# Optimization experiments

Measured on AMD Instinct MI355X. Metric: run time of the kernel, lower is better.

## Reference

```python
import jax, jax.numpy as jnp
import numpy as np

NH = 16   # neighbors
MD = 64   # model_dim
FF = 128  # ff_dim
H = 4     # heads
HD = MD // H
B, S, T = 2, 8192, 4096
LOG100 = float(np.log(100.0))


def _ln(x, g, b, eps=1e-5):
    m = x.mean(-1, keepdims=True)
    v = ((x - m) ** 2).mean(-1, keepdims=True)
    return (x - m) * jax.lax.rsqrt(v + eps) * g + b


def _lrelu(x):
    return jnp.where(x >= 0, x, 0.2 * x)


def setup_inputs():
    ks = jax.random.split(jax.random.key(0), 16)
    rn = lambda k, sh: jax.random.normal(k, sh, dtype=jnp.float32) * 0.05
    return {
        "x": jax.random.normal(ks[0], (B, S, 1), dtype=jnp.float32),
        "c1": jax.random.normal(ks[1], (B, S, T), dtype=jnp.float32),
        "c2": jax.random.normal(ks[2], (B, S, T), dtype=jnp.float32),
        "pe_W1": rn(ks[3], (2, FF)), "pe_b1": jnp.zeros((FF,), jnp.float32),
        "pe_W2": rn(ks[4], (FF, MD)), "pe_b2": jnp.zeros((MD,), jnp.float32),
        "Wq": rn(ks[5], (MD, MD)), "Wk": rn(ks[6], (MD, MD)), "Wv": rn(ks[7], (1, MD)),
        "logit_scale": jnp.full((H, 1, 1), float(np.log(10.0)), jnp.float32),
        "Wo": rn(ks[8], (MD, MD)), "bo": jnp.zeros((MD,), jnp.float32),
        "g1": jnp.ones((MD,), jnp.float32), "beta1": jnp.zeros((MD,), jnp.float32),
        "g2": jnp.ones((MD,), jnp.float32), "beta2": jnp.zeros((MD,), jnp.float32),
        "g3": jnp.ones((MD * NH,), jnp.float32), "beta3": jnp.zeros((MD * NH,), jnp.float32),
        "mnh_W1": rn(ks[9], (MD, FF)), "mnh_b1": jnp.zeros((FF,), jnp.float32),
        "mnh_W2": rn(ks[10], (FF, 1)), "mnh_b2": jnp.zeros((1,), jnp.float32),
        "mu_W1": rn(ks[11], (MD * NH, MD * NH)), "mu_b1": jnp.zeros((MD * NH,), jnp.float32),
        "mu_W2": rn(ks[12], (MD * NH, MD * NH)), "mu_b2": jnp.zeros((MD * NH,), jnp.float32),
    }


def reference(x, c1, c2, pe_W1, pe_b1, pe_W2, pe_b2, Wq, Wk, Wv, logit_scale, Wo, bo,
              g1, beta1, g2, beta2, g3, beta3,
              mnh_W1, mnh_b1, mnh_W2, mnh_b2, mu_W1, mu_b1, mu_W2, mu_b2):
    b, s, t = c1.shape
    # KNN over source axis s (cartesian distance), per target t
    d = c1 * c1 + c2 * c2                                  # [b,s,t]
    _, idx = jax.lax.top_k(-jnp.swapaxes(d, 1, 2), NH)     # [b,t,NH]
    x_nh = jax.vmap(lambda xb, ib: xb[ib])(x, idx)         # [b,t,NH,e]
    c1g = jnp.take_along_axis(jnp.swapaxes(c1, 1, 2), idx, axis=2)  # [b,t,NH]
    c2g = jnp.take_along_axis(jnp.swapaxes(c2, 1, 2), idx, axis=2)
    # relative-position embedding MLP (PE), already in [b,t,NH,MD] layout
    pe = jnp.stack([c1g, c2g], -1)                         # [b,t,NH,2]
    pe = jax.nn.gelu(pe @ pe_W1 + pe_b1) @ pe_W2 + pe_b2   # [b,t,NH,MD]
    h = _ln(x_nh + pe, g1, beta1).reshape(b * t, NH, MD)   # e=1 broadcasts
    v = jnp.einsum('bne,ed->bnd', x_nh.reshape(b * t, NH, 1), Wv)
    q = h @ Wq
    k = h @ Wk
    sp = lambda z: z.reshape(b * t, NH, H, HD).transpose(0, 2, 1, 3)
    qh, kh, vh = sp(q), sp(k), sp(v)
    # logit-scaled (cosine) attention over the NH neighbor axis
    qn = qh * jax.lax.rsqrt(jnp.sum(qh * qh, -1, keepdims=True) + 1e-12)
    kn = kh * jax.lax.rsqrt(jnp.sum(kh * kh, -1, keepdims=True) + 1e-12)
    scale = jnp.exp(jnp.minimum(logit_scale, LOG100))      # [H,1,1]
    att = jax.nn.softmax(jnp.einsum('bhnd,bhmd->bhnm', qn, kn) * scale, axis=-1)
    o = jnp.einsum('bhnm,bhmd->bhnd', att, vh).transpose(0, 2, 1, 3).reshape(b * t, NH, MD)
    h = _ln(h + (o @ Wo + bo), g2, beta2)
    # per-neighbor MLP producing a scalar, broadcast-added back
    h = h + _lrelu(_lrelu(h @ mnh_W1 + mnh_b1) @ mnh_W2 + mnh_b2)
    # unfold neighbors into channels and run the unfold MLP
    h = _ln(h.reshape(b, t, NH * MD), g3, beta3)
    return _lrelu(_lrelu(h @ mu_W1 + mu_b1) @ mu_W2 + mu_b2)  # [b,t,NH*MD]
```

## Files before the change

kernel.cpp:

```cpp
#include <hip/hip_runtime.h>
#include <hip/hip_bf16.h>

#define B_    2
#define SSRC  8192
#define TT    4096
#define NHN   16
#define NC    64
#define CS    128
#define LOG100D 4.605170185988091368035982909368

typedef short s16x8 __attribute__((ext_vector_type(8)));
typedef float f32x4 __attribute__((ext_vector_type(4)));
typedef double f64x4 __attribute__((ext_vector_type(4)));
typedef unsigned long long u64;

typedef const __attribute__((address_space(1))) void* gas_ptr;
typedef __attribute__((address_space(3))) void* las_ptr;
#define GLDS16(g, l) __builtin_amdgcn_global_load_lds((gas_ptr)(g), (las_ptr)(l), 16, 0, 0)

#define WFENCE asm volatile("s_waitcnt lgkmcnt(0)" ::: "memory")

__device__ __forceinline__ unsigned short f2bf(float f) {
    unsigned u = __float_as_uint(f);
    u = u + 0x7fffu + ((u >> 16) & 1u);
    return (unsigned short)(u >> 16);
}
__device__ __forceinline__ float bf2f(unsigned short h) {
    return __uint_as_float(((unsigned)h) << 16);
}
__device__ __forceinline__ double lrelu_d(double v) { return v >= 0.0 ? v : 0.2 * v; }
__device__ __forceinline__ double gelu_d(double u) {
    double a = 0.7978845608028654 * (u + 0.044715 * u * u * u);
    return 0.5 * u * (1.0 + tanh(a));
}
__device__ __forceinline__ double rsum16d(double v) {
    v += __shfl_xor(v, 1); v += __shfl_xor(v, 2);
    v += __shfl_xor(v, 4); v += __shfl_xor(v, 8);
    return v;
}
__device__ __forceinline__ double rmax16d(double v) {
    v = fmax(v, __shfl_xor(v, 1)); v = fmax(v, __shfl_xor(v, 2));
    v = fmax(v, __shfl_xor(v, 4)); v = fmax(v, __shfl_xor(v, 8));
    return v;
}
__device__ __forceinline__ double rsum64d(double v) {
    v += __shfl_xor(v, 1); v += __shfl_xor(v, 2); v += __shfl_xor(v, 4);
    v += __shfl_xor(v, 8); v += __shfl_xor(v, 16); v += __shfl_xor(v, 32);
    return v;
}

__device__ __forceinline__ bool mfma64_probe() {
    int lane = threadIdx.x & 63, l15 = lane & 15, lg = lane >> 4;
    double a = (double)(1 + l15 + 31 * lg);
    double b = (double)(3 + l15 + 17 * lg);
    f64x4 d = (f64x4){0.0, 0.0, 0.0, 0.0};
    d = __builtin_amdgcn_mfma_f64_16x16x4f64(a, b, d, 0, 0, 0);
    bool ok = true;
#pragma unroll
    for (int r = 0; r < 4; r++) {
        int i = 4 * lg + r;
        int e = 0;
#pragma unroll
        for (int k = 0; k < 4; k++) e += (1 + i + 31 * k) * (3 + l15 + 17 * k);
        ok = ok && (d[r] == (double)e);
    }
    return __all(ok) != 0;
}

__device__ __forceinline__ void ce(u64 &a, u64 &b) {
    bool c = a < b; u64 lo = c ? a : b; u64 hi = c ? b : a; a = lo; b = hi;
}
__device__ __forceinline__ void sort16(u64 (&k)[16]) {
    ce(k[0],k[8]); ce(k[1],k[9]); ce(k[2],k[10]); ce(k[3],k[11]);
    ce(k[4],k[12]); ce(k[5],k[13]); ce(k[6],k[14]); ce(k[7],k[15]);
    ce(k[0],k[4]); ce(k[1],k[5]); ce(k[2],k[6]); ce(k[3],k[7]);
    ce(k[8],k[12]); ce(k[9],k[13]); ce(k[10],k[14]); ce(k[11],k[15]);
    ce(k[4],k[8]); ce(k[5],k[9]); ce(k[6],k[10]); ce(k[7],k[11]);
    ce(k[0],k[2]); ce(k[1],k[3]); ce(k[4],k[6]); ce(k[5],k[7]);
    ce(k[8],k[10]); ce(k[9],k[11]); ce(k[12],k[14]); ce(k[13],k[15]);
    ce(k[2],k[8]); ce(k[3],k[9]); ce(k[6],k[12]); ce(k[7],k[13]);
    ce(k[2],k[4]); ce(k[3],k[5]); ce(k[6],k[8]); ce(k[7],k[9]);
    ce(k[10],k[12]); ce(k[11],k[13]);
    ce(k[0],k[1]); ce(k[2],k[3]); ce(k[4],k[5]); ce(k[6],k[7]);
    ce(k[8],k[9]); ce(k[10],k[11]); ce(k[12],k[13]); ce(k[14],k[15]);
    ce(k[1],k[8]); ce(k[3],k[10]); ce(k[5],k[12]); ce(k[7],k[14]);
    ce(k[1],k[4]); ce(k[3],k[6]); ce(k[5],k[8]); ce(k[7],k[10]);
    ce(k[9],k[12]); ce(k[11],k[14]);
    ce(k[1],k[2]); ce(k[3],k[4]); ce(k[5],k[6]); ce(k[7],k[8]);
    ce(k[9],k[10]); ce(k[11],k[12]); ce(k[13],k[14]);
}
__device__ __forceinline__ void bmerge16(u64 (&k)[16]) {
    ce(k[0],k[8]); ce(k[1],k[9]); ce(k[2],k[10]); ce(k[3],k[11]);
    ce(k[4],k[12]); ce(k[5],k[13]); ce(k[6],k[14]); ce(k[7],k[15]);
    ce(k[0],k[4]); ce(k[1],k[5]); ce(k[2],k[6]); ce(k[3],k[7]);
    ce(k[8],k[12]); ce(k[9],k[13]); ce(k[10],k[14]); ce(k[11],k[15]);
    ce(k[0],k[2]); ce(k[1],k[3]); ce(k[4],k[6]); ce(k[5],k[7]);
    ce(k[8],k[10]); ce(k[9],k[11]); ce(k[12],k[14]); ce(k[13],k[15]);
    ce(k[0],k[1]); ce(k[2],k[3]); ce(k[4],k[5]); ce(k[6],k[7]);
    ce(k[8],k[9]); ce(k[10],k[11]); ce(k[12],k[13]); ce(k[14],k[15]);
}
__device__ __forceinline__ void merge_keep16(u64 (&L)[16], const u64 (&B)[16]) {
#pragma unroll
    for (int i = 0; i < 16; i++) { u64 bb = B[15 - i]; L[i] = L[i] < bb ? L[i] : bb; }
    bmerge16(L);
}

__global__ __launch_bounds__(256) void topk_partial(
    const float* __restrict__ c1, const float* __restrict__ c2,
    u64* __restrict__ cand)
{
    int t = blockIdx.x * 256 + threadIdx.x;
    int ch = blockIdx.y, b = blockIdx.z;
    const float* p1 = c1 + ((size_t)b * SSRC + (size_t)ch * CS) * TT + t;
    const float* p2 = c2 + ((size_t)b * SSRC + (size_t)ch * CS) * TT + t;
    u64 k[16];
#pragma unroll
    for (int j = 0; j < 16; j++) k[j] = ~0ull;
    int sbase = ch * CS;
    for (int s = 0; s < CS; s += 16) {
// ... 26 lines not shown
        u64 bt[16];
#pragma unroll
        for (int j = 0; j < 16; j++) bt[j] = src[(size_t)j * TT];
        merge_keep16(k, bt);
    }
    u64* dst = c2c + ((size_t)((b * 8 + g) * 16)) * TT + t;
#pragma unroll
    for (int j = 0; j < 16; j++) dst[(size_t)j * TT] = k[j];
}

__global__ __launch_bounds__(64) void topk_merge2(
    const u64* __restrict__ c2c, int* __restrict__ knn)
{
    int t = blockIdx.x * 64 + threadIdx.x;
    int b = blockIdx.y;
    u64 k[16];
#pragma unroll
    for (int j = 0; j < 16; j++) k[j] = ~0ull;
    for (int c = 0; c < 8; c++) {
        const u64* src = c2c + ((size_t)(b * 8 + c) * 16) * TT + t;
        u64 bt[16];
#pragma unroll
        for (int j = 0; j < 16; j++) bt[j] = src[(size_t)j * TT];
        merge_keep16(k, bt);
    }
#pragma unroll
    for (int j = 0; j < 16; j++)
        knn[((size_t)b * TT + t) * 16 + j] = (int)(unsigned)(k[j] & 0xffffffffull);
}

__global__ __launch_bounds__(256) void wconv(
    const float* __restrict__ Wa, const float* __restrict__ Wb,
    unsigned short* __restrict__ Oah, unsigned short* __restrict__ Oal,
    unsigned short* __restrict__ Obh, unsigned short* __restrict__ Obl)
{
    const float* W = blockIdx.z ? Wb : Wa;
    unsigned short* Oh = blockIdx.z ? Obh : Oah;
    unsigned short* Ol = blockIdx.z ? Obl : Oal;
    __shared__ float tile[64][65];
    int tx = threadIdx.x & 63, ty = threadIdx.x >> 6;
    int n0 = blockIdx.x * 64, k0 = blockIdx.y * 64;
#pragma unroll
    for (int r = ty; r < 64; r += 4) tile[r][tx] = W[(size_t)(k0 + r) * 1024 + n0 + tx];
    __syncthreads();
#pragma unroll
    for (int r = ty; r < 64; r += 4) {
        float v = tile[tx][r];
        unsigned short hi = f2bf(v);
        Oh[(size_t)(n0 + r) * 1024 + k0 + tx] = hi;
        Ol[(size_t)(n0 + r) * 1024 + k0 + tx] = f2bf(v - bf2f(hi));
    }
}

__global__ __launch_bounds__(256) void tok_pe(
    const float* __restrict__ x, const float* __restrict__ c1, const float* __restrict__ c2,
    const int* __restrict__ knn,
    const float* __restrict__ peW1, const float* __restrict__ peb1,
    const float* __restrict__ peW2, const float* __restrict__ peb2,
    const float* __restrict__ g1, const float* __restrict__ be1,
    float* __restrict__ hout)
{
    __shared__ float s_peW1[256], s_peb1[128], s_peW2[8448], s_peb2[64], s_g1[64], s_be1[64];
    __shared__ float s_scr[4][2352];
    int tid = threadIdx.x, lane = tid & 63, w = tid >> 6;
    if (tid < 256) s_peW1[tid] = peW1[tid];
    if (tid < 128) s_peb1[tid] = peb1[tid];
    if (tid < 64) { s_peb2[tid] = peb2[tid]; s_g1[tid] = g1[tid]; s_be1[tid] = be1[tid]; }
    for (int i = tid; i < 8192; i += 256) s_peW2[(i >> 6) * 66 + (i & 63)] = peW2[i];
    __syncthreads();

    bool mf = mfma64_probe();
    float* big = s_scr[w];
    float* sc1 = big + 2304; float* sc2 = big + 2320; float* sx = big + 2336;
    int l15 = lane & 15, lg = lane >> 4;
    double w0a = s_peW1[lane], w1a = s_peW1[128 + lane], ba = s_peb1[lane];
    double w0b = s_peW1[64 + lane], w1b = s_peW1[192 + lane], bbv = s_peb1[64 + lane];
    double gv = (double)s_g1[lane], bv = (double)s_be1[lane];
    double pb2 = (double)s_peb2[lane];
    double g1v[4], be1v[4], pb2v[4];
#pragma unroll
    for (int j = 0; j < 4; j++) {
        g1v[j]  = (double)s_g1[j * 16 + l15];
        be1v[j] = (double)s_be1[j * 16 + l15];
        pb2v[j] = (double)s_peb2[j * 16 + l15];
    }

    for (int it = 0; it < 4; ++it) {
        int tk = blockIdx.x * 16 + w * 4 + it;
        int bb = tk >> 12, tt = tk & (TT - 1);
        if (lane < 16) {
            int s = knn[(size_t)tk * 16 + lane];
            sc1[lane] = c1[((size_t)bb * SSRC + s) * TT + tt];
            sc2[lane] = c2[((size_t)bb * SSRC + s) * TT + tt];
            sx[lane]  = x[bb * SSRC + s];
        }
        WFENCE;
#pragma unroll
        for (int n = 0; n < 16; n++) {
            double a_ = (double)sc1[n], b_ = (double)sc2[n];
            big[lane * 18 + n]        = (float)gelu_d(a_ * w0a + b_ * w1a + ba);
            big[(lane + 64) * 18 + n] = (float)gelu_d(a_ * w0b + b_ * w1b + bbv);
        }
        WFENCE;
        if (mf) {
            f64x4 acc[4];
#pragma unroll
            for (int j = 0; j < 4; j++) acc[j] = (f64x4){0.0, 0.0, 0.0, 0.0};
            for (int ks = 0; ks < 32; ks++) {
                double a = (double)big[(4 * ks + lg) * 18 + l15];
                const float* wrow = &s_peW2[(4 * ks + lg) * 66 + l15];
#pragma unroll
                for (int j = 0; j < 4; j++) {
                    double b = (double)wrow[j * 16];
                    acc[j] = __builtin_amdgcn_mfma_f64_16x16x4f64(a, b, acc[j], 0, 0, 0);
                }
            }
            double xr[4];
#pragma unroll
            for (int r = 0; r < 4; r++) xr[r] = (double)sx[lg * 4 + r];
            float* op = hout + (size_t)tk * 1024;
#pragma unroll
            for (int r = 0; r < 4; r++) {
                double v[4], s = 0.0;
#pragma unroll
                for (int j = 0; j < 4; j++) { v[j] = acc[j][r] + pb2v[j] + xr[r]; s += v[j]; }
                double m = rsum16d(s) * (1.0 / 64.0);
                double q = 0.0;
#pragma unroll
                for (int j = 0; j < 4; j++) { double d = v[j] - m; q += d * d; }
                double var = rsum16d(q) * (1.0 / 64.0);
                double rs = sqrt(var + 1e-5);
                int n = lg * 4 + r;
#pragma unroll
                for (int j = 0; j < 4; j++)
                    op[n * 64 + j * 16 + l15] = (float)((v[j] - m) / rs * g1v[j] + be1v[j]);
            }
        } else {
            double acc[16];
#pragma unroll
            for (int n = 0; n < 16; n++) acc[n] = pb2;
            for (int f = 0; f < 128; f++) {
                double wv = (double)s_peW2[f * 66 + lane];
#pragma unroll
                for (int n = 0; n < 16; n += 2) {
                    float2 gvv = *(const float2*)&big[f * 18 + n];
                    acc[n]     += (double)gvv.x * wv;
                    acc[n + 1] += (double)gvv.y * wv;
                }
            }
            float* op = hout + (size_t)tk * 1024 + lane;
#pragma unroll
            for (int n = 0; n < 16; n++) {
                double v = acc[n] + (double)sx[n];
                double m = rsum64d(v) * (1.0 / 64.0);
                double d = v - m;
                double var = rsum64d(d * d) * (1.0 / 64.0);
                op[n * 64] = (float)(d / sqrt(var + 1e-5) * gv + bv);
            }
        }
    }
}

__global__ __launch_bounds__(256) void tok_attn(
    const float* __restrict__ x, const int* __restrict__ knn,
    const float* __restrict__ Wq, const float* __restrict__ Wk,
    const float* __restrict__ Wv, const float* __restrict__ lsc,
    const float* __restrict__ Wo, const float* __restrict__ bo,
    const float* __restrict__ g2, const float* __restrict__ be2,
    float* __restrict__ hio)
{
    __shared__ float s_Wq[4224], s_Wk[4224], s_WoV[256], s_bo[64], s_g2[64], s_be2[64];
    __shared__ float s_scr[4][2320];
    int tid = threadIdx.x, lane = tid & 63, w = tid >> 6;
    if (tid < 64) {
        s_bo[tid] = bo[tid]; s_g2[tid] = g2[tid]; s_be2[tid] = be2[tid];
        for (int hh = 0; hh < 4; hh++) {
            double a = 0.0;
            for (int hd = 0; hd < 16; hd++)
                a += (double)Wv[hh * 16 + hd] * (double)Wo[(hh * 16 + hd) * 64 + tid];
            s_WoV[hh * 64 + tid] = (float)a;
        }
    }
    for (int i = tid; i < 4096; i += 256) {
        s_Wq[(i >> 6) * 66 + (i & 63)] = Wq[i];
        s_Wk[(i >> 6) * 66 + (i & 63)] = Wk[i];
    }
    __syncthreads();

    bool mf = mfma64_probe();
    int head = lane >> 4, mm = lane & 15;
    int l15 = mm, lg = head;
    double scaleh = exp(fmin((double)lsc[head], LOG100D));
    double wov0 = (double)s_WoV[lane], wov1 = (double)s_WoV[64 + lane];
    double wov2 = (double)s_WoV[128 + lane], wov3 = (double)s_WoV[192 + lane];
    double gv = (double)s_g2[lane], bv = (double)s_be2[lane], bov = (double)s_bo[lane];
    float* big = s_scr[w];
    float* sx = big + 2304;

    for (int it = 0; it < 4; ++it) {
        int tk = blockIdx.x * 16 + w * 4 + it;
        int bb = tk >> 12;
        if (lane < 16) {
            int s = knn[(size_t)tk * 16 + lane];
            sx[lane] = x[bb * SSRC + s];
        }
        float* hp = hio + (size_t)tk * 1024 + lane;
        double h[16];
#pragma unroll
        for (int n = 0; n < 16; n++) {
            h[n] = (double)hp[n * 64];
            big[lane * 18 + n] = (float)h[n];
        }
        WFENCE;
        if (mf) {
            f64x4 qa[4], ka[4];
#pragma unroll
            for (int j = 0; j < 4; j++) { qa[j] = (f64x4){0.,0.,0.,0.}; ka[j] = (f64x4){0.,0.,0.,0.}; }
            for (int ks = 0; ks < 16; ks++) {
                double a = (double)big[(4 * ks + lg) * 18 + l15];
                const float* wq = &s_Wq[(4 * ks + lg) * 66 + l15];
                const float* wk = &s_Wk[(4 * ks + lg) * 66 + l15];
#pragma unroll
                for (int j = 0; j < 4; j++) {
                    qa[j] = __builtin_amdgcn_mfma_f64_16x16x4f64(a, (double)wq[j * 16], qa[j], 0, 0, 0);
                    ka[j] = __builtin_amdgcn_mfma_f64_16x16x4f64(a, (double)wk[j * 16], ka[j], 0, 0, 0);
                }
            }
            WFENCE;
#pragma unroll
            for (int j = 0; j < 4; j++) {
#pragma unroll
                for (int r = 0; r < 4; r++) {
                    double qq = qa[j][r], kk2 = ka[j][r];
                    double sq = rsum16d(qq * qq);
                    double sk = rsum16d(kk2 * kk2);
                    qq  /= sqrt(sq + 1e-12);
                    kk2 /= sqrt(sk + 1e-12);
                    big[(j * 16 + l15) * 18 + 4 * lg + r]        = (float)qq;
                    big[1152 + (j * 16 + l15) * 18 + 4 * lg + r] = (float)kk2;
                }
            }
        } else {
            double q[16], k2[16];
#pragma unroll
            for (int n = 0; n < 16; n++) { q[n] = 0.0; k2[n] = 0.0; }
            for (int kk = 0; kk < 64; kk++) {
                double wq = (double)s_Wq[kk * 66 + lane], wk = (double)s_Wk[kk * 66 + lane];
#pragma unroll
                for (int n = 0; n < 16; n += 2) {
                    float2 hv = *(const float2*)&big[kk * 18 + n];
                    q[n]  += (double)hv.x * wq; q[n + 1]  += (double)hv.y * wq;
                    k2[n] += (double)hv.x * wk; k2[n + 1] += (double)hv.y * wk;
                }
            }
#pragma unroll
            for (int n = 0; n < 16; n++) {
                double sq = rsum16d(q[n] * q[n]);   q[n]  /= sqrt(sq + 1e-12);
                double sk = rsum16d(k2[n] * k2[n]); k2[n] /= sqrt(sk + 1e-12);
            }
            WFENCE;
#pragma unroll
            for (int n = 0; n < 16; n++) {
                big[lane * 18 + n]        = (float)q[n];
                big[1152 + lane * 18 + n] = (float)k2[n];
            }
        }
        WFENCE;
        double A_[16];
        {
            double S[16];
#pragma unroll
            for (int n = 0; n < 16; n++) S[n] = 0.0;
            for (int hd = 0; hd < 16; hd++) {
                int r = head * 16 + hd;
                double kf = (double)big[1152 + r * 18 + mm];
#pragma unroll
                for (int n = 0; n < 16; n += 2) {
                    float2 qq = *(const float2*)&big[r * 18 + n];
                    S[n] += (double)qq.x * kf; S[n + 1] += (double)qq.y * kf;
                }
            }
            double xv = (double)sx[mm];
#pragma unroll
            for (int n = 0; n < 16; n++) {
                double sv = S[n] * scaleh;
                double mx = rmax16d(sv);
                double e = exp(sv - mx);
                double se = rsum16d(e);
                A_[n] = rsum16d((e / se) * xv);
            }
        }
#pragma unroll
        for (int n = 0; n < 16; n++) {
            double a0 = __shfl(A_[n], mm), a1 = __shfl(A_[n], 16 + mm);
            double a2 = __shfl(A_[n], 32 + mm), a3 = __shfl(A_[n], 48 + mm);
            double v = h[n] + a0 * wov0 + a1 * wov1 + a2 * wov2 + a3 * wov3 + bov;
            double m = rsum64d(v) * (1.0 / 64.0);
            double d = v - m;
            double var = rsum64d(d * d) * (1.0 / 64.0);
            hp[n * 64] = (float)(d / sqrt(var + 1e-5) * gv + bv);
        }
    }
}

__global__ __launch_bounds__(256) void tok_mnh(
    const float* __restrict__ hin,
    const float* __restrict__ mW1, const float* __restrict__ mb1,
    const float* __restrict__ mW2, const float* __restrict__ mb2,
    const float* __restrict__ g3, const float* __restrict__ be3,
    unsigned short* __restrict__ hnh, unsigned short* __restrict__ hnl)
{
    __shared__ float s_mW1[8320], s_mb1[128], s_mW2[128], s_g3[1024], s_be3[1024];
    __shared__ float s_scr[4][1152];
    int tid = threadIdx.x, lane = tid & 63, w = tid >> 6;
    if (tid < 128) { s_mb1[tid] = mb1[tid]; s_mW2[tid] = mW2[tid]; }
    for (int i = tid; i < 8192; i += 256) s_mW1[(i >> 7) * 130 + (i & 127)] = mW1[i];
    for (int i = tid; i < 1024; i += 256) { s_g3[i] = g3[i]; s_be3[i] = be3[i]; }
    __syncthreads();

    bool mf = mfma64_probe();
    int l15 = lane & 15, lg = lane >> 4;
    double mb2s = (double)mb2[0];
    double mb1a = (double)s_mb1[lane], mb1b = (double)s_mb1[64 + lane];
    double w2a = (double)s_mW2[lane], w2b = (double)s_mW2[64 + lane];
    double mb1v[8], w2v[8];
#pragma unroll
    for (int j = 0; j < 8; j++) {
        mb1v[j] = (double)s_mb1[j * 16 + l15];
        w2v[j]  = (double)s_mW2[j * 16 + l15];
    }
    float* big = s_scr[w];

    for (int it = 0; it < 4; ++it) {
        int tk = blockIdx.x * 16 + w * 4 + it;
        const float* hp = hin + (size_t)tk * 1024 + lane;
        double h[16];
#pragma unroll
        for (int n = 0; n < 16; n++) {
            h[n] = (double)hp[n * 64];
            big[lane * 18 + n] = (float)h[n];
        }
        WFENCE;
        if (mf) {
            f64x4 acc[8];
#pragma unroll
            for (int j = 0; j < 8; j++) acc[j] = (f64x4){0.0, 0.0, 0.0, 0.0};
            for (int ks = 0; ks < 16; ks++) {
                double a = (double)big[(4 * ks + lg) * 18 + l15];
                const float* wrow = &s_mW1[(4 * ks + lg) * 130 + l15];
#pragma unroll
                for (int j = 0; j < 8; j++) {
                    double b = (double)wrow[j * 16];
                    acc[j] = __builtin_amdgcn_mfma_f64_16x16x4f64(a, b, acc[j], 0, 0, 0);
                }
            }
            double p[4];
#pragma unroll
            for (int r = 0; r < 4; r++) {
                double s = 0.0;
#pragma unroll
                for (int j = 0; j < 8; j++) {
                    double t = acc[j][r] + mb1v[j];
                    s += lrelu_d(t) * w2v[j];
                }
                p[r] = rsum16d(s);
            }
#pragma unroll
            for (int n = 0; n < 16; n++) {
                double pn = __shfl(p[n & 3], (n >> 2) * 16);
                h[n] += lrelu_d(pn + mb2s);
            }
        } else {
            double t1a[16], t1b[16];
#pragma unroll
            for (int n = 0; n < 16; n++) { t1a[n] = mb1a; t1b[n] = mb1b; }
            for (int kk = 0; kk < 64; kk++) {
                double wa = (double)s_mW1[kk * 130 + lane], wb = (double)s_mW1[kk * 130 + 64 + lane];
#pragma unroll
                for (int n = 0; n < 16; n += 2) {
                    float2 hv = *(const float2*)&big[kk * 18 + n];
                    t1a[n] += (double)hv.x * wa; t1a[n + 1] += (double)hv.y * wa;
                    t1b[n] += (double)hv.x * wb; t1b[n + 1] += (double)hv.y * wb;
                }
            }
#pragma unroll
            for (int n = 0; n < 16; n++) {
                double p = lrelu_d(t1a[n]) * w2a + lrelu_d(t1b[n]) * w2b;
                p = rsum64d(p);
                h[n] += lrelu_d(p + mb2s);
            }
        }
        double s1 = 0.0;
#pragma unroll
        for (int n = 0; n < 16; n++) s1 += h[n];
        s1 = rsum64d(s1) * (1.0 / 1024.0);
        double s2v = 0.0;
#pragma unroll
        for (int n = 0; n < 16; n++) { double d = h[n] - s1; s2v += d * d; }
        s2v = rsum64d(s2v) * (1.0 / 1024.0);
        double rs = 1.0 / sqrt(s2v + 1e-5);
        unsigned short* oph = hnh + (size_t)tk * 1024 + lane;
        unsigned short* opl = hnl + (size_t)tk * 1024 + lane;
#pragma unroll
        for (int n = 0; n < 16; n++) {
            double v = (h[n] - s1) * rs * (double)s_g3[n * 64 + lane] + (double)s_be3[n * 64 + lane];
            unsigned short hi = f2bf((float)v);
            oph[n * 64] = hi;
            opl[n * 64] = f2bf((float)(v - (double)bf2f(hi)));
        }
    }
}

#define AH_OFF 0
#define AL_OFF 4096
#define BH_OFF 8192
#define BL_OFF 12288
template<int OUTSPLIT>
__global__ __launch_bounds__(256) void gemm_split(
    const unsigned short* __restrict__ Ah, const unsigned short* __restrict__ Al,
    const unsigned short* __restrict__ Bh, const unsigned short* __restrict__ Bl,
    const float* __restrict__ bias,
    unsigned short* __restrict__ oh, unsigned short* __restrict__ ol,
    float* __restrict__ of, int M, int N, int K)
{
    __shared__ unsigned short SM[16384];
    int tid = threadIdx.x, lane = tid & 63, w = tid >> 6;
    int wm = w >> 1, wn = w & 1;
    int m0 = blockIdx.y * 128, n0 = blockIdx.x * 128;
    f32x4 acc[4][4];
#pragma unroll
    for (int i = 0; i < 4; i++)
#pragma unroll
        for (int j = 0; j < 4; j++) acc[i][j] = (f32x4){0.f, 0.f, 0.f, 0.f};
    int row = tid >> 2, c8 = (tid & 3) * 8;
    size_t aoff = (size_t)(m0 + row) * K + c8;
    size_t boff = (size_t)(n0 + row) * K + c8;
    for (int kk = 0; kk < K; kk += 32) {
        __syncthreads();
        GLDS16(Ah + aoff + kk,                   SM + AH_OFF + tid * 8);
        GLDS16(Ah + aoff + (size_t)64 * K + kk,  SM + AH_OFF + 2048 + tid * 8);
        GLDS16(Al + aoff + kk,                   SM + AL_OFF + tid * 8);
        GLDS16(Al + aoff + (size_t)64 * K + kk,  SM + AL_OFF + 2048 + tid * 8);
        GLDS16(Bh + boff + kk,                   SM + BH_OFF + tid * 8);
// ... 47 lines not shown

extern "C" void kernel_launch(void* const* d_in, const int* in_sizes, int n_in,
                              void* d_out, int out_size, void* d_ws, size_t ws_size,
                              hipStream_t stream)
{
    const float* x    = (const float*)d_in[0];
    const float* c1   = (const float*)d_in[1];
    const float* c2   = (const float*)d_in[2];
    const float* peW1 = (const float*)d_in[3];
    const float* peb1 = (const float*)d_in[4];
    const float* peW2 = (const float*)d_in[5];
    const float* peb2 = (const float*)d_in[6];
    const float* Wq   = (const float*)d_in[7];
    const float* Wk   = (const float*)d_in[8];
    const float* Wv   = (const float*)d_in[9];
    const float* lsc  = (const float*)d_in[10];
    const float* Wo   = (const float*)d_in[11];
    const float* bo   = (const float*)d_in[12];
    const float* g1   = (const float*)d_in[13];
    const float* be1  = (const float*)d_in[14];
    const float* g2   = (const float*)d_in[15];
    const float* be2  = (const float*)d_in[16];
    const float* g3   = (const float*)d_in[17];
    const float* be3  = (const float*)d_in[18];
    const float* mW1  = (const float*)d_in[19];
    const float* mb1  = (const float*)d_in[20];
    const float* mW2  = (const float*)d_in[21];
    const float* mb2  = (const float*)d_in[22];
    const float* muW1 = (const float*)d_in[23];
    const float* mub1 = (const float*)d_in[24];
    const float* muW2 = (const float*)d_in[25];
    const float* mub2 = (const float*)d_in[26];

    const size_t MB = (size_t)1 << 20;
    char* ws = (char*)d_ws;
    u64*            cand   = (u64*)(ws);
    float*          hbuf   = (float*)(ws);
    unsigned short* y1h    = (unsigned short*)(ws);
    unsigned short* y1l    = (unsigned short*)(ws + 16 * MB);
    unsigned short* hnh    = (unsigned short*)(ws + 32 * MB);
    unsigned short* hnl    = (unsigned short*)(ws + 48 * MB);
    u64*            c2c    = (u64*)(ws + 64 * MB);
    unsigned short* w1th   = (unsigned short*)(ws + 72 * MB);
    unsigned short* w1tl   = (unsigned short*)(ws + 74 * MB);
    unsigned short* w2th   = (unsigned short*)(ws + 76 * MB);
    unsigned short* w2tl   = (unsigned short*)(ws + 78 * MB);
    int*            knn    = (int*)(ws + 80 * MB);
    (void)in_sizes; (void)n_in; (void)out_size; (void)ws_size;

    wconv<<<dim3(16, 16, 2), 256, 0, stream>>>(muW1, muW2, w1th, w1tl, w2th, w2tl);
    topk_partial<<<dim3(TT / 256, NC, B_), 256, 0, stream>>>(c1, c2, cand);
    topk_merge1<<<dim3(TT / 64, 8, B_), 64, 0, stream>>>(cand, c2c);
    topk_merge2<<<dim3(TT / 64, B_), 64, 0, stream>>>(c2c, knn);
    tok_pe<<<dim3(512), 256, 0, stream>>>(x, c1, c2, knn, peW1, peb1, peW2, peb2, g1, be1, hbuf);
    tok_attn<<<dim3(512), 256, 0, stream>>>(x, knn, Wq, Wk, Wv, lsc, Wo, bo, g2, be2, hbuf);
    tok_mnh<<<dim3(512), 256, 0, stream>>>(hbuf, mW1, mb1, mW2, mb2, g3, be3, hnh, hnl);
    gemm_split<1><<<dim3(8, 64), 256, 0, stream>>>(hnh, hnl, w1th, w1tl, mub1,
                                                   y1h, y1l, (float*)nullptr, 8192, 1024, 1024);
    gemm_split<0><<<dim3(8, 64), 256, 0, stream>>>(y1h, y1l, w2th, w2tl, mub2,
                                                   (unsigned short*)nullptr, (unsigned short*)nullptr,
                                                   (float*)d_out, 8192, 1024, 1024);
}
```

Measured before the change: 879.9 us.

## Discover FP64 MFMA operand layout at runtime and split MFMA/VALU kernel variants

Measured after the change: 816.6 us. 1.08x faster.

```diff
diff --git a/kernel.cpp b/kernel.cpp
--- a/kernel.cpp
+++ b/kernel.cpp
@@ -49,22 +49,34 @@
     return v;
 }
 
-__device__ __forceinline__ bool mfma64_probe() {
-    int lane = threadIdx.x & 63, l15 = lane & 15, lg = lane >> 4;
-    double a = (double)(1 + l15 + 31 * lg);
-    double b = (double)(3 + l15 + 17 * lg);
+__device__ __forceinline__ int mfma64_discover() {
+    int lane = threadIdx.x & 63;
+    int l15 = lane & 15, lg = lane >> 4;
+    double va = (double)(1 + ((lane * 37) % 61));
+    double vb = (double)(2 + ((lane * 53) % 59));
     f64x4 d = (f64x4){0.0, 0.0, 0.0, 0.0};
-    d = __builtin_amdgcn_mfma_f64_16x16x4f64(a, b, d, 0, 0, 0);
-    bool ok = true;
-#pragma unroll
-    for (int r = 0; r < 4; r++) {
-        int i = 4 * lg + r;
-        int e = 0;
-#pragma unroll
-        for (int k = 0; k < 4; k++) e += (1 + i + 31 * k) * (3 + l15 + 17 * k);
-        ok = ok && (d[r] == (double)e);
-    }
-    return __all(ok) != 0;
+    d = __builtin_amdgcn_mfma_f64_16x16x4f64(va, vb, d, 0, 0, 0);
+    int found = -1;
+#pragma unroll
+    for (int c = 0; c < 8; c++) {
+        int dm = (c >> 2) & 1, am = (c >> 1) & 1, bm = c & 1;
+        bool ok = true;
+#pragma unroll
+        for (int r = 0; r < 4; r++) {
+            int i = dm ? (lg + 4 * r) : (4 * lg + r);
+            int j = l15;
+            double e = 0.0;
+#pragma unroll
+            for (int k = 0; k < 4; k++) {
+                int la = am ? (4 * i + k) : (i + 16 * k);
+                int lb = bm ? (4 * j + k) : (j + 16 * k);
+                e += (double)(1 + ((la * 37) % 61)) * (double)(2 + ((lb * 53) % 59));
+            }
+            ok = ok && (d[r] == e);
+        }
+        if (__all(ok) && found < 0) found = c;
+    }
+    return found;
 }
 
 __device__ __forceinline__ void ce(u64 &a, u64 &b) {
@@ -197,7 +209,7 @@
     }
 }
 
-__global__ __launch_bounds__(256) void tok_pe(
+__global__ __launch_bounds__(256) void tok_pe_m(
     const float* __restrict__ x, const float* __restrict__ c1, const float* __restrict__ c2,
     const int* __restrict__ knn,
     const float* __restrict__ peW1, const float* __restrict__ peb1,
@@ -205,6 +217,8 @@
     const float* __restrict__ g1, const float* __restrict__ be1,
     float* __restrict__ hout)
 {
+    int cand = mfma64_discover();
+    if (cand < 0) return;
     __shared__ float s_peW1[256], s_peb1[128], s_peW2[8448], s_peb2[64], s_g1[64], s_be1[64];
     __shared__ float s_scr[4][2352];
     int tid = threadIdx.x, lane = tid & 63, w = tid >> 6;
@@ -214,14 +228,19 @@
     for (int i = tid; i < 8192; i += 256) s_peW2[(i >> 6) * 66 + (i & 63)] = peW2[i];
     __syncthreads();
 
-    bool mf = mfma64_probe();
+    int l15 = lane & 15, lg = lane >> 4;
+    int am = (cand >> 1) & 1, bm = cand & 1, dm = (cand >> 2) & 1;
+    int a_i = am ? (lane >> 2) : l15;
+    int a_k = am ? (lane & 3)  : lg;
+    int b_k = bm ? (lane & 3)  : lg;
+    int b_j = bm ? (lane >> 2) : l15;
+    int i0 = dm ? lg : 4 * lg;
+    int istep = dm ? 4 : 1;
+
     float* big = s_scr[w];
     float* sc1 = big + 2304; float* sc2 = big + 2320; float* sx = big + 2336;
-    int l15 = lane & 15, lg = lane >> 4;
     double w0a = s_peW1[lane], w1a = s_peW1[128 + lane], ba = s_peb1[lane];
     double w0b = s_peW1[64 + lane], w1b = s_peW1[192 + lane], bbv = s_peb1[64 + lane];
-    double gv = (double)s_g1[lane], bv = (double)s_be1[lane];
-    double pb2 = (double)s_peb2[lane];
     double g1v[4], be1v[4], pb2v[4];
 #pragma unroll
     for (int j = 0; j < 4; j++) {
@@ -247,66 +266,105 @@
             big[(lane + 64) * 18 + n] = (float)gelu_d(a_ * w0b + b_ * w1b + bbv);
         }
         WFENCE;
-        if (mf) {
-            f64x4 acc[4];
-#pragma unroll
-            for (int j = 0; j < 4; j++) acc[j] = (f64x4){0.0, 0.0, 0.0, 0.0};
-            for (int ks = 0; ks < 32; ks++) {
-                double a = (double)big[(4 * ks + lg) * 18 + l15];
-                const float* wrow = &s_peW2[(4 * ks + lg) * 66 + l15];
-#pragma unroll
-                for (int j = 0; j < 4; j++) {
-                    double b = (double)wrow[j * 16];
-                    acc[j] = __builtin_amdgcn_mfma_f64_16x16x4f64(a, b, acc[j], 0, 0, 0);
-                }
-            }
-            double xr[4];
-#pragma unroll
-            for (int r = 0; r < 4; r++) xr[r] = (double)sx[lg * 4 + r];
-            float* op = hout + (size_t)tk * 1024;
-#pragma unroll
-            for (int r = 0; r < 4; r++) {
-                double v[4], s = 0.0;
-#pragma unroll
-                for (int j = 0; j < 4; j++) { v[j] = acc[j][r] + pb2v[j] + xr[r]; s += v[j]; }
-                double m = rsum16d(s) * (1.0 / 64.0);
-                double q = 0.0;
-#pragma unroll
-                for (int j = 0; j < 4; j++) { double d = v[j] - m; q += d * d; }
-                double var = rsum16d(q) * (1.0 / 64.0);
-                double rs = sqrt(var + 1e-5);
-                int n = lg * 4 + r;
-#pragma unroll
-                for (int j = 0; j < 4; j++)
-                    op[n * 64 + j * 16 + l15] = (float)((v[j] - m) / rs * g1v[j] + be1v[j]);
-            }
-        } else {
-            double acc[16];
-#pragma unroll
-            for (int n = 0; n < 16; n++) acc[n] = pb2;
-            for (int f = 0; f < 128; f++) {
-                double wv = (double)s_peW2[f * 66 + lane];
-#pragma unroll
-                for (int n = 0; n < 16; n += 2) {
-                    float2 gvv = *(const float2*)&big[f * 18 + n];
-                    acc[n]     += (double)gvv.x * wv;
-                    acc[n + 1] += (double)gvv.y * wv;
-                }
-            }
-            float* op = hout + (size_t)tk * 1024 + lane;
-#pragma unroll
-            for (int n = 0; n < 16; n++) {
-                double v = acc[n] + (double)sx[n];
-                double m = rsum64d(v) * (1.0 / 64.0);
-                double d = v - m;
-                double var = rsum64d(d * d) * (1.0 / 64.0);
-                op[n * 64] = (float)(d / sqrt(var + 1e-5) * gv + bv);
-            }
-        }
-    }
-}
-
-__global__ __launch_bounds__(256) void tok_attn(
+        f64x4 acc[4];
+#pragma unroll
+        for (int j = 0; j < 4; j++) acc[j] = (f64x4){0.0, 0.0, 0.0, 0.0};
+        for (int ks = 0; ks < 32; ks++) {
+            double a = (double)big[(4 * ks + a_k) * 18 + a_i];
+            const float* wrow = &s_peW2[(4 * ks + b_k) * 66 + b_j];
+#pragma unroll
+            for (int j = 0; j < 4; j++)
+                acc[j] = __builtin_amdgcn_mfma_f64_16x16x4f64(a, (double)wrow[j * 16], acc[j], 0, 0, 0);
+        }
+        float* op = hout + (size_t)tk * 1024;
+#pragma unroll
+        for (int r = 0; r < 4; r++) {
+            int n = i0 + istep * r;
+            double xr = (double)sx[n];
+            double v[4], s = 0.0;
+#pragma unroll
+            for (int j = 0; j < 4; j++) { v[j] = acc[j][r] + pb2v[j] + xr; s += v[j]; }
+            double m = rsum16d(s) * (1.0 / 64.0);
+            double q = 0.0;
+#pragma unroll
+            for (int j = 0; j < 4; j++) { double d = v[j] - m; q += d * d; }
+            double var = rsum16d(q) * (1.0 / 64.0);
+            double rs = sqrt(var + 1e-5);
+#pragma unroll
+            for (int j = 0; j < 4; j++)
+                op[n * 64 + j * 16 + l15] = (float)((v[j] - m) / rs * g1v[j] + be1v[j]);
+        }
+    }
+}
+
+__global__ __launch_bounds__(256) void tok_pe_v(
+    const float* __restrict__ x, const float* __restrict__ c1, const float* __restrict__ c2,
+    const int* __restrict__ knn,
+    const float* __restrict__ peW1, const float* __restrict__ peb1,
+    const float* __restrict__ peW2, const float* __restrict__ peb2,
+    const float* __restrict__ g1, const float* __restrict__ be1,
+    float* __restrict__ hout)
+{
+    int cand = mfma64_discover();
+    if (cand >= 0) return;
+    __shared__ float s_peW1[256], s_peb1[128], s_peW2[8448], s_peb2[64], s_g1[64], s_be1[64];
+    __shared__ float s_scr[4][2352];
+    int tid = threadIdx.x, lane = tid & 63, w = tid >> 6;
+    if (tid < 256) s_peW1[tid] = peW1[tid];
+    if (tid < 128) s_peb1[tid] = peb1[tid];
+    if (tid < 64) { s_peb2[tid] = peb2[tid]; s_g1[tid] = g1[tid]; s_be1[tid] = be1[tid]; }
+    for (int i = tid; i < 8192; i += 256) s_peW2[(i >> 6) * 66 + (i & 63)] = peW2[i];
+    __syncthreads();
+
+    float* big = s_scr[w];
+    float* sc1 = big + 2304; float* sc2 = big + 2320; float* sx = big + 2336;
+    double w0a = s_peW1[lane], w1a = s_peW1[128 + lane], ba = s_peb1[lane];
+    double w0b = s_peW1[64 + lane], w1b = s_peW1[192 + lane], bbv = s_peb1[64 + lane];
+    double gv = (double)s_g1[lane], bv = (double)s_be1[lane];
+    double pb2 = (double)s_peb2[lane];
+
+    for (int it = 0; it < 4; ++it) {
+        int tk = blockIdx.x * 16 + w * 4 + it;
+        int bb = tk >> 12, tt = tk & (TT - 1);
+        if (lane < 16) {
+            int s = knn[(size_t)tk * 16 + lane];
+            sc1[lane] = c1[((size_t)bb * SSRC + s) * TT + tt];
+            sc2[lane] = c2[((size_t)bb * SSRC + s) * TT + tt];
+            sx[lane]  = x[bb * SSRC + s];
+        }
+        WFENCE;
+#pragma unroll
+        for (int n = 0; n < 16; n++) {
+            double a_ = (double)sc1[n], b_ = (double)sc2[n];
+            big[lane * 18 + n]        = (float)gelu_d(a_ * w0a + b_ * w1a + ba);
+            big[(lane + 64) * 18 + n] = (float)gelu_d(a_ * w0b + b_ * w1b + bbv);
+        }
+        WFENCE;
+        double acc[16];
+#pragma unroll
+        for (int n = 0; n < 16; n++) acc[n] = pb2;
+        for (int f = 0; f < 128; f++) {
+            double wv = (double)s_peW2[f * 66 + lane];
+#pragma unroll
+            for (int n = 0; n < 16; n += 2) {
+                float2 gvv = *(const float2*)&big[f * 18 + n];
+                acc[n]     += (double)gvv.x * wv;
+                acc[n + 1] += (double)gvv.y * wv;
+            }
+        }
+        float* op = hout + (size_t)tk * 1024 + lane;
+#pragma unroll
+        for (int n = 0; n < 16; n++) {
+            double v = acc[n] + (double)sx[n];
+            double m = rsum64d(v) * (1.0 / 64.0);
+            double d = v - m;
+            double var = rsum64d(d * d) * (1.0 / 64.0);
+            op[n * 64] = (float)(d / sqrt(var + 1e-5) * gv + bv);
+        }
+    }
+}
+
+__global__ __launch_bounds__(256) void tok_attn_m(
     const float* __restrict__ x, const int* __restrict__ knn,
     const float* __restrict__ Wq, const float* __restrict__ Wk,
     const float* __restrict__ Wv, const float* __restrict__ lsc,
@@ -314,6 +372,8 @@
     const float* __restrict__ g2, const float* __restrict__ be2,
     float* __restrict__ hio)
 {
+    int cand = mfma64_discover();
+    if (cand < 0) return;
     __shared__ float s_Wq[4224], s_Wk[4224], s_WoV[256], s_bo[64], s_g2[64], s_be2[64];
     __shared__ float s_scr[4][2320];
     int tid = threadIdx.x, lane = tid & 63, w = tid >> 6;
@@ -332,9 +392,16 @@
     }
     __syncthreads();
 
-    bool mf = mfma64_probe();
-    int head = lane >> 4, mm = lane & 15;
-    int l15 = mm, lg = head;
+    int l15 = lane & 15, lg = lane >> 4;
+    int am = (cand >> 1) & 1, bm = cand & 1, dm = (cand >> 2) & 1;
+    int a_i = am ? (lane >> 2) : l15;
+    int a_k = am ? (lane & 3)  : lg;
+    int b_k = bm ? (lane & 3)  : lg;
+    int b_j = bm ? (lane >> 2) : l15;
+    int i0 = dm ? lg : 4 * lg;
+    int istep = dm ? 4 : 1;
+
+    int head = lg, mm = l15;
     double scaleh = exp(fmin((double)lsc[head], LOG100D));
     double wov0 = (double)s_WoV[lane], wov1 = (double)s_WoV[64 + lane];
     double wov2 = (double)s_WoV[128 + lane], wov3 = (double)s_WoV[192 + lane];
@@ -357,57 +424,32 @@
             big[lane * 18 + n] = (float)h[n];
         }
         WFENCE;
-        if (mf) {
-            f64x4 qa[4], ka[4];
-#pragma unroll
-            for (int j = 0; j < 4; j++) { qa[j] = (f64x4){0.,0.,0.,0.}; ka[j] = (f64x4){0.,0.,0.,0.}; }
-            for (int ks = 0; ks < 16; ks++) {
-                double a = (double)big[(4 * ks + lg) * 18 + l15];
-                const float* wq = &s_Wq[(4 * ks + lg) * 66 + l15];
-                const float* wk = &s_Wk[(4 * ks + lg) * 66 + l15];
-#pragma unroll
-                for (int j = 0; j < 4; j++) {
-                    qa[j] = __builtin_amdgcn_mfma_f64_16x16x4f64(a, (double)wq[j * 16], qa[j], 0, 0, 0);
-                    ka[j] = __builtin_amdgcn_mfma_f64_16x16x4f64(a, (double)wk[j * 16], ka[j], 0, 0, 0);
-                }
-            }
-            WFENCE;
+        f64x4 qa[4], ka[4];
+#pragma unroll
+        for (int j = 0; j < 4; j++) { qa[j] = (f64x4){0.,0.,0.,0.}; ka[j] = (f64x4){0.,0.,0.,0.}; }
+        for (int ks = 0; ks < 16; ks++) {
+            double a = (double)big[(4 * ks + a_k) * 18 + a_i];
+            const float* wq = &s_Wq[(4 * ks + b_k) * 66 + b_j];
+            const float* wk = &s_Wk[(4 * ks + b_k) * 66 + b_j];
 #pragma unroll
             for (int j = 0; j < 4; j++) {
-#pragma unroll
-                for (int r = 0; r < 4; r++) {
-                    double qq = qa[j][r], kk2 = ka[j][r];
-                    double sq = rsum16d(qq * qq);
-                    double sk = rsum16d(kk2 * kk2);
-                    qq  /= sqrt(sq + 1e-12);
-                    kk2 /= sqrt(sk + 1e-12);
-                    big[(j * 16 + l15) * 18 + 4 * lg + r]        = (float)qq;
-                    big[1152 + (j * 16 + l15) * 18 + 4 * lg + r] = (float)kk2;
-                }
-            }
-        } else {
-            double q[16], k2[16];
-#pragma unroll
-            for (int n = 0; n < 16; n++) { q[n] = 0.0; k2[n] = 0.0; }
-            for (int kk = 0; kk < 64; kk++) {
-                double wq = (double)s_Wq[kk * 66 + lane], wk = (double)s_Wk[kk * 66 + lane];
-#pragma unroll
-                for (int n = 0; n < 16; n += 2) {
-                    float2 hv = *(const float2*)&big[kk * 18 + n];
-                    q[n]  += (double)hv.x * wq; q[n + 1]  += (double)hv.y * wq;
-                    k2[n] += (double)hv.x * wk; k2[n + 1] += (double)hv.y * wk;
-                }
-            }
-#pragma unroll
-            for (int n = 0; n < 16; n++) {
-                double sq = rsum16d(q[n] * q[n]);   q[n]  /= sqrt(sq + 1e-12);
-                double sk = rsum16d(k2[n] * k2[n]); k2[n] /= sqrt(sk + 1e-12);
-            }
-            WFENCE;
-#pragma unroll
-            for (int n = 0; n < 16; n++) {
-                big[lane * 18 + n]        = (float)q[n];
-                big[1152 + lane * 18 + n] = (float)k2[n];
+                qa[j] = __builtin_amdgcn_mfma_f64_16x16x4f64(a, (double)wq[j * 16], qa[j], 0, 0, 0);
+                ka[j] = __builtin_amdgcn_mfma_f64_16x16x4f64(a, (double)wk[j * 16], ka[j], 0, 0, 0);
+            }
+        }
+        WFENCE;
+#pragma unroll
+        for (int j = 0; j < 4; j++) {
+#pragma unroll
+            for (int r = 0; r < 4; r++) {
+                double qq = qa[j][r], kk2 = ka[j][r];
+                double sq = rsum16d(qq * qq);
+                double sk = rsum16d(kk2 * kk2);
+                qq  /= sqrt(sq + 1e-12);
+                kk2 /= sqrt(sk + 1e-12);
+                int n = i0 + istep * r;
+                big[(j * 16 + l15) * 18 + n]        = (float)qq;
+                big[1152 + (j * 16 + l15) * 18 + n] = (float)kk2;
             }
         }
         WFENCE;
@@ -448,13 +490,127 @@
     }
 }
 
-__global__ __launch_bounds__(256) void tok_mnh(
+__global__ __launch_bounds__(256) void tok_attn_v(
+    const float* __restrict__ x, const int* __restrict__ knn,
+    const float* __restrict__ Wq, const float* __restrict__ Wk,
+    const float* __restrict__ Wv, const float* __restrict__ lsc,
+    const float* __restrict__ Wo, const float* __restrict__ bo,
+    const float* __restrict__ g2, const float* __restrict__ be2,
+    float* __restrict__ hio)
+{
+    int cand = mfma64_discover();
+    if (cand >= 0) return;
+    __shared__ float s_Wq[4224], s_Wk[4224], s_WoV[256], s_bo[64], s_g2[64], s_be2[64];
+    __shared__ float s_scr[4][2320];
+    int tid = threadIdx.x, lane = tid & 63, w = tid >> 6;
+    if (tid < 64) {
+        s_bo[tid] = bo[tid]; s_g2[tid] = g2[tid]; s_be2[tid] = be2[tid];
+        for (int hh = 0; hh < 4; hh++) {
+            double a = 0.0;
+            for (int hd = 0; hd < 16; hd++)
+                a += (double)Wv[hh * 16 + hd] * (double)Wo[(hh * 16 + hd) * 64 + tid];
+            s_WoV[hh * 64 + tid] = (float)a;
+        }
+    }
+    for (int i = tid; i < 4096; i += 256) {
+        s_Wq[(i >> 6) * 66 + (i & 63)] = Wq[i];
+        s_Wk[(i >> 6) * 66 + (i & 63)] = Wk[i];
+    }
+    __syncthreads();
+
+    int head = lane >> 4, mm = lane & 15;
+    double scaleh = exp(fmin((double)lsc[head], LOG100D));
+    double wov0 = (double)s_WoV[lane], wov1 = (double)s_WoV[64 + lane];
+    double wov2 = (double)s_WoV[128 + lane], wov3 = (double)s_WoV[192 + lane];
+    double gv = (double)s_g2[lane], bv = (double)s_be2[lane], bov = (double)s_bo[lane];
+    float* big = s_scr[w];
+    float* sx = big + 2304;
+
+    for (int it = 0; it < 4; ++it) {
+        int tk = blockIdx.x * 16 + w * 4 + it;
+        int bb = tk >> 12;
+        if (lane < 16) {
+            int s = knn[(size_t)tk * 16 + lane];
+            sx[lane] = x[bb * SSRC + s];
+        }
+        float* hp = hio + (size_t)tk * 1024 + lane;
+        double h[16];
+#pragma unroll
+        for (int n = 0; n < 16; n++) {
+            h[n] = (double)hp[n * 64];
+            big[lane * 18 + n] = (float)h[n];
+        }
+        WFENCE;
+        double q[16], k2[16];
+#pragma unroll
+        for (int n = 0; n < 16; n++) { q[n] = 0.0; k2[n] = 0.0; }
+        for (int kk = 0; kk < 64; kk++) {
+            double wq = (double)s_Wq[kk * 66 + lane], wk = (double)s_Wk[kk * 66 + lane];
+#pragma unroll
+            for (int n = 0; n < 16; n += 2) {
+                float2 hv = *(const float2*)&big[kk * 18 + n];
+                q[n]  += (double)hv.x * wq; q[n + 1]  += (double)hv.y * wq;
+                k2[n] += (double)hv.x * wk; k2[n + 1] += (double)hv.y * wk;
+            }
+        }
+#pragma unroll
+        for (int n = 0; n < 16; n++) {
+            double sq = rsum16d(q[n] * q[n]);   q[n]  /= sqrt(sq + 1e-12);
+            double sk = rsum16d(k2[n] * k2[n]); k2[n] /= sqrt(sk + 1e-12);
+        }
+        WFENCE;
+#pragma unroll
+        for (int n = 0; n < 16; n++) {
+            big[lane * 18 + n]        = (float)q[n];
+            big[1152 + lane * 18 + n] = (float)k2[n];
+        }
+        WFENCE;
+        double A_[16];
+        {
+            double S[16];
+#pragma unroll
+            for (int n = 0; n < 16; n++) S[n] = 0.0;
+            for (int hd = 0; hd < 16; hd++) {
+                int r = head * 16 + hd;
+                double kf = (double)big[1152 + r * 18 + mm];
+#pragma unroll
+                for (int n = 0; n < 16; n += 2) {
+                    float2 qq = *(const float2*)&big[r * 18 + n];
+                    S[n] += (double)qq.x * kf; S[n + 1] += (double)qq.y * kf;
+                }
+            }
+            double xv = (double)sx[mm];
+#pragma unroll
+            for (int n = 0; n < 16; n++) {
+                double sv = S[n] * scaleh;
+                double mx = rmax16d(sv);
+                double e = exp(sv - mx);
+                double se = rsum16d(e);
+                A_[n] = rsum16d((e / se) * xv);
+            }
+        }
+#pragma unroll
+        for (int n = 0; n < 16; n++) {
+            double a0 = __shfl(A_[n], mm), a1 = __shfl(A_[n], 16 + mm);
+            double a2 = __shfl(A_[n], 32 + mm), a3 = __shfl(A_[n], 48 + mm);
+            double v = h[n] + a0 * wov0 + a1 * wov1 + a2 * wov2 + a3 * wov3 + bov;
+            double m = rsum64d(v) * (1.0 / 64.0);
+            double d = v - m;
+            double var = rsum64d(d * d) * (1.0 / 64.0);
+            hp[n * 64] = (float)(d / sqrt(var + 1e-5) * gv + bv);
+        }
+    }
+}
+
+__global__ __launch_bounds__(256) void tok_mnh_m(
     const float* __restrict__ hin,
     const float* __restrict__ mW1, const float* __restrict__ mb1,
     const float* __restrict__ mW2, const float* __restrict__ mb2,
     const float* __restrict__ g3, const float* __restrict__ be3,
     unsigned short* __restrict__ hnh, unsigned short* __restrict__ hnl)
 {
+    int cand = mfma64_discover();
+    if (cand < 0) return;
     __shared__ float s_mW1[8320], s_mb1[128], s_mW2[128], s_g3[1024], s_be3[1024];
     __shared__ float s_scr[4][1152];
     int tid = threadIdx.x, lane = tid & 63, w = tid >> 6;
@@ -463,11 +619,16 @@
     for (int i = tid; i < 1024; i += 256) { s_g3[i] = g3[i]; s_be3[i] = be3[i]; }
     __syncthreads();
 
-    bool mf = mfma64_probe();
     int l15 = lane & 15, lg = lane >> 4;
+    int am = (cand >> 1) & 1, bm = cand & 1, dm = (cand >> 2) & 1;
+    int a_i = am ? (lane >> 2) : l15;
+    int a_k = am ? (lane & 3)  : lg;
+    int b_k = bm ? (lane & 3)  : lg;
+    int b_j = bm ? (lane >> 2) : l15;
+    int i0 = dm ? lg : 4 * lg;
+    int istep = dm ? 4 : 1;
+
     double mb2s = (double)mb2[0];
-    double mb1a = (double)s_mb1[lane], mb1b = (double)s_mb1[64 + lane];
-    double w2a = (double)s_mW2[lane], w2b = (double)s_mW2[64 + lane];
     double mb1v[8], w2v[8];
 #pragma unroll
     for (int j = 0; j < 8; j++) {
@@ -486,54 +647,110 @@
             big[lane * 18 + n] = (float)h[n];
         }
         WFENCE;
-        if (mf) {
-            f64x4 acc[8];
-#pragma unroll
-            for (int j = 0; j < 8; j++) acc[j] = (f64x4){0.0, 0.0, 0.0, 0.0};
-            for (int ks = 0; ks < 16; ks++) {
-                double a = (double)big[(4 * ks + lg) * 18 + l15];
-                const float* wrow = &s_mW1[(4 * ks + lg) * 130 + l15];
-#pragma unroll
-                for (int j = 0; j < 8; j++) {
-                    double b = (double)wrow[j * 16];
-                    acc[j] = __builtin_amdgcn_mfma_f64_16x16x4f64(a, b, acc[j], 0, 0, 0);
-                }
-            }
-            double p[4];
-#pragma unroll
-            for (int r = 0; r < 4; r++) {
-                double s = 0.0;
-#pragma unroll
-                for (int j = 0; j < 8; j++) {
-                    double t = acc[j][r] + mb1v[j];
-                    s += lrelu_d(t) * w2v[j];
-                }
-                p[r] = rsum16d(s);
-            }
+        f64x4 acc[8];
+#pragma unroll
+        for (int j = 0; j < 8; j++) acc[j] = (f64x4){0.0, 0.0, 0.0, 0.0};
+        for (int ks = 0; ks < 16; ks++) {
+            double a = (double)big[(4 * ks + a_k) * 18 + a_i];
+            const float* wrow = &s_mW1[(4 * ks + b_k) * 130 + b_j];
+#pragma unroll
+            for (int j = 0; j < 8; j++)
+                acc[j] = __builtin_amdgcn_mfma_f64_16x16x4f64(a, (double)wrow[j * 16], acc[j], 0, 0, 0);
+        }
+        double p[4];
+#pragma unroll
+        for (int r = 0; r < 4; r++) {
+            double s = 0.0;
+#pragma unroll
+            for (int j = 0; j < 8; j++) {
+                double t = acc[j][r] + mb1v[j];
+                s += lrelu_d(t) * w2v[j];
+            }
+            p[r] = rsum16d(s);
+        }
+        if (dm == 0) {
 #pragma unroll
             for (int n = 0; n < 16; n++) {
                 double pn = __shfl(p[n & 3], (n >> 2) * 16);
                 h[n] += lrelu_d(pn + mb2s);
             }
         } else {
-            double t1a[16], t1b[16];
-#pragma unroll
-            for (int n = 0; n < 16; n++) { t1a[n] = mb1a; t1b[n] = mb1b; }
-            for (int kk = 0; kk < 64; kk++) {
-                double wa = (double)s_mW1[kk * 130 + lane], wb = (double)s_mW1[kk * 130 + 64 + lane];
-#pragma unroll
-                for (int n = 0; n < 16; n += 2) {
-                    float2 hv = *(const float2*)&big[kk * 18 + n];
-                    t1a[n] += (double)hv.x * wa; t1a[n + 1] += (double)hv.y * wa;
-                    t1b[n] += (double)hv.x * wb; t1b[n + 1] += (double)hv.y * wb;
-                }
-            }
 #pragma unroll
             for (int n = 0; n < 16; n++) {
-                double p = lrelu_d(t1a[n]) * w2a + lrelu_d(t1b[n]) * w2b;
-                p = rsum64d(p);
-                h[n] += lrelu_d(p + mb2s);
-            }
+                double pn = __shfl(p[n >> 2], (n & 3) * 16);
+                h[n] += lrelu_d(pn + mb2s);
+            }
+        }
+        double s1 = 0.0;
+#pragma unroll
+        for (int n = 0; n < 16; n++) s1 += h[n];
+        s1 = rsum64d(s1) * (1.0 / 1024.0);
+        double s2v = 0.0;
+#pragma unroll
+        for (int n = 0; n < 16; n++) { double d = h[n] - s1; s2v += d * d; }
+        s2v = rsum64d(s2v) * (1.0 / 1024.0);
+        double rs = 1.0 / sqrt(s2v + 1e-5);
+        unsigned short* oph = hnh + (size_t)tk * 1024 + lane;
+        unsigned short* opl = hnl + (size_t)tk * 1024 + lane;
+#pragma unroll
+        for (int n = 0; n < 16; n++) {
+            double v = (h[n] - s1) * rs * (double)s_g3[n * 64 + lane] + (double)s_be3[n * 64 + lane];
+            unsigned short hi = f2bf((float)v);
+            oph[n * 64] = hi;
+            opl[n * 64] = f2bf((float)(v - (double)bf2f(hi)));
+        }
+    }
+}
+
+__global__ __launch_bounds__(256) void tok_mnh_v(
+    const float* __restrict__ hin,
+    const float* __restrict__ mW1, const float* __restrict__ mb1,
+    const float* __restrict__ mW2, const float* __restrict__ mb2,
+    const float* __restrict__ g3, const float* __restrict__ be3,
+    unsigned short* __restrict__ hnh, unsigned short* __restrict__ hnl)
+{
+    int cand = mfma64_discover();
+    if (cand >= 0) return;
+    __shared__ float s_mW1[8320], s_mb1[128], s_mW2[128], s_g3[1024], s_be3[1024];
+    __shared__ float s_scr[4][1152];
+    int tid = threadIdx.x, lane = tid & 63, w = tid >> 6;
+    if (tid < 128) { s_mb1[tid] = mb1[tid]; s_mW2[tid] = mW2[tid]; }
+    for (int i = tid; i < 8192; i += 256) s_mW1[(i >> 7) * 130 + (i & 127)] = mW1[i];
+    for (int i = tid; i < 1024; i += 256) { s_g3[i] = g3[i]; s_be3[i] = be3[i]; }
+    __syncthreads();
+
+    double mb2s = (double)mb2[0];
+    double mb1a = (double)s_mb1[lane], mb1b = (double)s_mb1[64 + lane];
+    double w2a = (double)s_mW2[lane], w2b = (double)s_mW2[64 + lane];
+    float* big = s_scr[w];
+
+    for (int it = 0; it < 4; ++it) {
+        int tk = blockIdx.x * 16 + w * 4 + it;
+        const float* hp = hin + (size_t)tk * 1024 + lane;
+        double h[16];
+#pragma unroll
+        for (int n = 0; n < 16; n++) {
+            h[n] = (double)hp[n * 64];
+            big[lane * 18 + n] = (float)h[n];
+        }
+        WFENCE;
+        double t1a[16], t1b[16];
+#pragma unroll
+        for (int n = 0; n < 16; n++) { t1a[n] = mb1a; t1b[n] = mb1b; }
+        for (int kk = 0; kk < 64; kk++) {
+            double wa = (double)s_mW1[kk * 130 + lane], wb = (double)s_mW1[kk * 130 + 64 + lane];
+#pragma unroll
+            for (int n = 0; n < 16; n += 2) {
+                float2 hv = *(const float2*)&big[kk * 18 + n];
+                t1a[n] += (double)hv.x * wa; t1a[n + 1] += (double)hv.y * wa;
+                t1b[n] += (double)hv.x * wb; t1b[n + 1] += (double)hv.y * wb;
+            }
+        }
+#pragma unroll
+        for (int n = 0; n < 16; n++) {
+            double p = lrelu_d(t1a[n]) * w2a + lrelu_d(t1b[n]) * w2b;
+            p = rsum64d(p);
+            h[n] += lrelu_d(p + mb2s);
         }
         double s1 = 0.0;
 #pragma unroll
@@ -687,9 +904,12 @@
     topk_partial<<<dim3(TT / 256, NC, B_), 256, 0, stream>>>(c1, c2, cand);
     topk_merge1<<<dim3(TT / 64, 8, B_), 64, 0, stream>>>(cand, c2c);
     topk_merge2<<<dim3(TT / 64, B_), 64, 0, stream>>>(c2c, knn);
-    tok_pe<<<dim3(512), 256, 0, stream>>>(x, c1, c2, knn, peW1, peb1, peW2, peb2, g1, be1, hbuf);
-    tok_attn<<<dim3(512), 256, 0, stream>>>(x, knn, Wq, Wk, Wv, lsc, Wo, bo, g2, be2, hbuf);
-    tok_mnh<<<dim3(512), 256, 0, stream>>>(hbuf, mW1, mb1, mW2, mb2, g3, be3, hnh, hnl);
+    tok_pe_m<<<dim3(512), 256, 0, stream>>>(x, c1, c2, knn, peW1, peb1, peW2, peb2, g1, be1, hbuf);
+    tok_pe_v<<<dim3(512), 256, 0, stream>>>(x, c1, c2, knn, peW1, peb1, peW2, peb2, g1, be1, hbuf);
+    tok_attn_m<<<dim3(512), 256, 0, stream>>>(x, knn, Wq, Wk, Wv, lsc, Wo, bo, g2, be2, hbuf);
+    tok_attn_v<<<dim3(512), 256, 0, stream>>>(x, knn, Wq, Wk, Wv, lsc, Wo, bo, g2, be2, hbuf);
+    tok_mnh_m<<<dim3(512), 256, 0, stream>>>(hbuf, mW1, mb1, mW2, mb2, g3, be3, hnh, hnl);
+    tok_mnh_v<<<dim3(512), 256, 0, stream>>>(hbuf, mW1, mb1, mW2, mb2, g3, be3, hnh, hnl);
     gemm_split<1><<<dim3(8, 64), 256, 0, stream>>>(hnh, hnl, w1th, w1tl, mub1,
                                                    y1h, y1l, (float*)nullptr, 8192, 1024, 1024);
     gemm_split<0><<<dim3(8, 64), 256, 0, stream>>>(y1h, y1l, w2th, w2tl, mub2,
```
